# Kernel optimization log

Measured on AMD Instinct MI355X. Metric: run time of the kernel, lower is better.

The kernel has to match this reference:

```python
import jax, jax.numpy as jnp
import numpy as np

N_NODES = 100000
N_EDGES = 1600000


def _sage_conv(x, src, dst, W_l, W_r, b):
    """PyG SAGEConv (mean aggr): lin_l(mean of neighbor feats) + b + lin_r(x)."""
    n = x.shape[0]
    msgs = x[src]                                            # [E, F] gather
    agg = jax.ops.segment_sum(msgs, dst, num_segments=n)     # [N, F]
    cnt = jax.ops.segment_sum(jnp.ones((src.shape[0],), x.dtype), dst,
                              num_segments=n)                # [N]
    mean = agg / jnp.maximum(cnt, 1.0)[:, None]
    return mean @ W_l + b + x @ W_r


def setup_inputs() -> dict:
    key = jax.random.key(0)
    ks = jax.random.split(key, 8)
    x = jax.random.normal(ks[0], (N_NODES, 64), dtype=jnp.float32)
    edge_index = jax.random.randint(ks[1], (2, N_EDGES), 0, N_NODES, dtype=jnp.int64)
    # Glorot-ish small init for weights
    W1_l = jax.random.normal(ks[2], (64, 128), dtype=jnp.float32) * 0.1
    W1_r = jax.random.normal(ks[3], (64, 128), dtype=jnp.float32) * 0.1
    b1 = jax.random.normal(ks[4], (128,), dtype=jnp.float32) * 0.1
    W2_l = jax.random.normal(ks[5], (128, 64), dtype=jnp.float32) * 0.1
    W2_r = jax.random.normal(ks[6], (128, 64), dtype=jnp.float32) * 0.1
    b2 = jax.random.normal(ks[7], (64,), dtype=jnp.float32) * 0.1
    return {"x": x, "edge_index": edge_index, "W1_l": W1_l, "W1_r": W1_r,
            "b1": b1, "W2_l": W2_l, "W2_r": W2_r, "b2": b2}


def reference(x, edge_index, W1_l, W1_r, b1, W2_l, W2_r, b2):
    src, dst = edge_index[0], edge_index[1]
    h = jax.nn.relu(_sage_conv(x, src, dst, W1_l, W1_r, b1))  # [N, 128]
    out = _sage_conv(h, src, dst, W2_l, W2_r, b2)             # [N, 64]
    return out
```

## Files before the change

kernel.cpp:

```cpp
#include <hip/hip_runtime.h>
#include <hip/hip_bf16.h>
#include <stdint.h>


typedef unsigned short u16;
typedef __attribute__((ext_vector_type(8))) short short8;
typedef __attribute__((ext_vector_type(4))) float f32x4;

#define BSHIFT 9
#define BSIZE  512
#define CHUNK  8192
#define NBP    512
#define NCMAX  256

__device__ __forceinline__ float bf2f(u16 v) { return __uint_as_float(((uint32_t)v) << 16); }
__device__ __forceinline__ float bfu_lo(uint32_t u) { return __uint_as_float(u << 16); }
__device__ __forceinline__ float bfu_hi(uint32_t u) { return __uint_as_float(u & 0xffff0000u); }
__device__ __forceinline__ u16 f2bf(float f) {
    uint32_t u = __float_as_uint(f);
    return (u16)((u + 0x7fffu + ((u >> 16) & 1u)) >> 16);
}

__device__ __forceinline__ int wave_scan(int v) {
    int lane = threadIdx.x & 63;
#pragma unroll
    for (int d = 1; d < 64; d <<= 1) {
        int t = __shfl_up(v, d);
        if (lane >= d) v += t;
    }
    return v;
}

__device__ __forceinline__ int block_scan512(int v, int* ws, int* ptot) {
    int tid = threadIdx.x, lane = tid & 63, wid = tid >> 6;
    int s = wave_scan(v);
    if (lane == 63) ws[wid] = s;
    __syncthreads();
    int add = 0, tot = 0;
#pragma unroll
    for (int w = 0; w < 8; w++) { int x = ws[w]; tot += x; if (w < wid) add += x; }
    if (ptot) *ptot = tot;
    __syncthreads();
    return s + add;
}

__global__ __launch_bounds__(512) void setup_k(
    const void* __restrict__ x, const void* __restrict__ ei,
    const void* __restrict__ W1l, const void* __restrict__ W1r,
    const void* __restrict__ b1, const void* __restrict__ W2l,
    const void* __restrict__ W2r, const void* __restrict__ b2,
    u16* __restrict__ wpk, u16* __restrict__ xb,
    int* __restrict__ hist2d, int* __restrict__ flags,
    int nn, int ne, int nb, int nchunk, int ncvt,
    int c0, int c1, int c2, int c3, int c4, int c5, int c6) {
    __shared__ int sh[512];
    __shared__ int sflag;
    int bid = blockIdx.x, tid = threadIdx.x;
    if (bid < nchunk) {
        sh[tid] = 0;
        int samp = 0;
        if (tid < 32) {
            long long n32 = 2LL * ne;
            long long stride = n32 / 32; if (stride < 1) stride = 1;
            long long i = (long long)tid * stride; i |= 1;
            if (i >= n32) i = 1;
            samp = (((const int*)ei)[i] != 0);
        }
        unsigned long long m = __ballot(samp);
        if (tid == 0) sflag = (m == 0ULL) ? 1 : 0;
        __syncthreads();
        int e64 = sflag;
        int base = bid * CHUNK;
#pragma unroll
        for (int j = 0; j < 16; j++) {
            int e = base + j * 512 + tid;
            if (e < ne) {
                int dst = e64 ? (int)((const long long*)ei)[(size_t)ne + e]
                              : ((const int*)ei)[(size_t)ne + e];
                if ((unsigned)dst < (unsigned)nn) atomicAdd(&sh[dst >> BSHIFT], 1);
            }
        }
        __syncthreads();
        if (tid < NBP) hist2d[bid * NBP + tid] = (tid < nb) ? sh[tid] : 0;
    } else if (bid < nchunk + ncvt) {
        int samp = 0;
        if (tid < 32) {
            int C = c0; int stride = C / 32; if (stride < 1) stride = 1;
            long long i = (long long)tid * stride;
            if (i > C - 1) i = C - 1; i &= ~1LL;
            u16 v = ((const u16*)x)[i];
            int e = (v >> 7) & 0xFF;
            samp = ((e >= 0x50 && e <= 0x97) || v == 0) ? 1 : 0;
        }
        unsigned long long m = __ballot(samp);
        if (tid == 0) sflag = (__popcll(m) >= 24) ? 1 : 0;
        __syncthreads();
        if (sflag) return;
        int i = (bid - nchunk) * 512 + tid;
        if (i < nn * 16) {
            float4 f = ((const float4*)x)[i];
            *(ushort4*)&xb[(size_t)i * 4] =
                make_ushort4(f2bf(f.x), f2bf(f.y), f2bf(f.z), f2bf(f.w));
        }
    } else if (bid < nchunk + ncvt + 4) {
        int b = bid - nchunk - ncvt;
        const void* src = (b == 0) ? W1l : (b == 1) ? W1r : (b == 2) ? W2l : W2r;
        int C = (b == 0) ? c1 : (b == 1) ? c2 : (b == 2) ? c4 : c5;
        int samp = 0;
        if (tid < 32) {
            int stride = C / 32; if (stride < 1) stride = 1;
            long long i = (long long)tid * stride;
            if (i > C - 1) i = C - 1; i &= ~1LL;
            u16 v = ((const u16*)src)[i];
            int e = (v >> 7) & 0xFF;
            samp = ((e >= 0x50 && e <= 0x97) || v == 0) ? 1 : 0;
        }
        unsigned long long m = __ballot(samp);
        if (tid == 0) sflag = (__popcll(m) >= 24) ? 1 : 0;
        __syncthreads();
        int isbf = sflag;
        u16* dst = wpk + ((b >= 2) ? (16384 + (b - 2) * 8192) : 0);
        for (int i = tid; i < 2048; i += 512) {
            u16 v0, v1, v2, v3;
            if (isbf) {
                ushort4 u = ((const ushort4*)src)[i];
                v0 = u.x; v1 = u.y; v2 = u.z; v3 = u.w;
            } else {
                float4 u = ((const float4*)src)[i];
                v0 = f2bf(u.x); v1 = f2bf(u.y); v2 = f2bf(u.z); v3 = f2bf(u.w);
            }
            int k, n, k8;
            if (b <= 1) { k = i >> 5; n = (i & 31) * 4; k8 = (b == 1 ? 8 : 0) + (k >> 3); }
            else        { k = i >> 4; n = (i & 15) * 4; k8 = k >> 3; }
            int kc = k8 >> 2, q = k8 & 3, w = k & 7;
            int basei = ((n >> 4) * 4 + kc) * 512 + (q * 16 + (n & 15)) * 8 + w;
            dst[basei] = v0; dst[basei + 8] = v1; dst[basei + 16] = v2; dst[basei + 24] = v3;
        }
    } else {
        int a = tid >> 5, lane = tid & 31;
        if (tid < 8) sh[tid] = 0;
        __syncthreads();
        if (a < 7) {
            const void* ptrs[7] = {x, W1l, W1r, b1, W2l, W2r, b2};
            int cs[7] = {c0, c1, c2, c3, c4, c5, c6};
            int C = cs[a];
            int stride = C / 32; if (stride < 1) stride = 1;
            long long i = (long long)lane * stride;
            if (i > C - 1) i = C - 1;
            i &= ~1LL;
            u16 v = ((const u16*)ptrs[a])[i];
            int e = (v >> 7) & 0xFF;
            int sane = ((e >= 0x50 && e <= 0x97) || v == 0) ? 1 : 0;
            atomicAdd(&sh[a], sane);
        } else if (a == 7) {
            long long n32 = 2LL * ne;
            long long stride = n32 / 32; if (stride < 1) stride = 1;
            long long i = (long long)lane * stride; i |= 1;
            if (i >= n32) i = 1;
            int wv = ((const int*)ei)[i];
            atomicAdd(&sh[7], wv != 0 ? 1 : 0);
        }
        __syncthreads();
        if (tid < 7) flags[tid] = (sh[tid] >= 24) ? 1 : 0;
        if (tid == 7) flags[7] = (sh[7] == 0) ? 1 : 0;
    }
}

__global__ __launch_bounds__(512) void partition_k(
    const void* __restrict__ ei, const int* __restrict__ hist2d,
    unsigned* __restrict__ ep, int nn, int ne, int nb, int nchunk) {
    __shared__ unsigned stage[CHUNK];
    __shared__ u16 ab[CHUNK];
    __shared__ int hist[512], exl[512], gbase[512], lcur[512];
    __shared__ int ws[8];
    __shared__ int e64s;
    int tid = threadIdx.x;
    int base = blockIdx.x * CHUNK;
    hist[tid] = 0;
    int samp = 0;
    if (tid < 32) {
        long long n32 = 2LL * ne;
        long long stride = n32 / 32; if (stride < 1) stride = 1;
        long long i = (long long)tid * stride; i |= 1;
        if (i >= n32) i = 1;
        samp = (((const int*)ei)[i] != 0);
    }
    unsigned long long bm = __ballot(samp);
    if (tid == 0) e64s = (bm == 0ULL) ? 1 : 0;
    __syncthreads();
    int e64 = e64s;
    unsigned pk[16]; int bk[16];
#pragma unroll
    for (int j = 0; j < 16; j++) {
        int e = base + j * 512 + tid;
        bk[j] = -1;
        pk[j] = 0;
        if (e < ne) {
            int src, dst;
            if (e64) {
                src = (int)((const long long*)ei)[e];
                dst = (int)((const long long*)ei)[(size_t)ne + e];
            } else {
                src = ((const int*)ei)[e];
                dst = ((const int*)ei)[(size_t)ne + e];
            }
            if ((unsigned)dst < (unsigned)nn) {
                if ((unsigned)src >= (unsigned)nn) src = 0;
                bk[j] = dst >> BSHIFT;
                pk[j] = (unsigned)src | ((unsigned)(dst & (BSIZE - 1)) << 17);
                atomicAdd(&hist[bk[j]], 1);
            }
        }
    }
    __syncthreads();
    int hv = hist[tid];
    int tot;
    int inc1 = block_scan512(hv, ws, &tot);
    int ex = inc1 - hv;
    exl[tid] = ex;
    lcur[tid] = ex;
    int baseb = 0, tbt = 0;
    int mybid = blockIdx.x;
    if (tid < nb) {
        for (int c = 0; c < nchunk; c++) {
            int h = hist2d[c * NBP + tid];
            tbt += h;
            if (c < mybid) baseb += h;
        }
    }
    int inc2 = block_scan512(tbt, ws, nullptr);
    int bo_t = inc2 - tbt;
    gbase[tid] = (tid < nb) ? (bo_t + baseb) : 0;
    __syncthreads();
#pragma unroll
    for (int j = 0; j < 16; j++) {
        if (bk[j] >= 0) {
            int r = atomicAdd(&lcur[bk[j]], 1);
            stage[r] = pk[j];
            ab[r] = (u16)bk[j];
        }
    }
    __syncthreads();
    for (int j = tid; j < tot; j += 512) {
        int b = ab[j];
        ep[gbase[b] + (j - exl[b])] = stage[j];
    }
}

__global__ __launch_bounds__(512) void csr_fill2(
    const unsigned* __restrict__ ep, const int* __restrict__ hist2d,
    int* __restrict__ off, int* __restrict__ cnt, int* __restrict__ esrc,
    int nn, int nb, int nchunk) {
    __shared__ int hist[BSIZE], lcur[BSIZE];
    __shared__ int ws[8];
    __shared__ int s_end, s_cnt;
    int b = blockIdx.x;
    int tid = threadIdx.x;
    int tbt = 0;
    if (tid < nb) {
        for (int c = 0; c < nchunk; c++) tbt += hist2d[c * NBP + tid];
    }
    int incb = block_scan512(tbt, ws, nullptr);
    if (tid == b) { s_end = incb; s_cnt = tbt; }
    hist[tid] = 0;
    __syncthreads();
    int end = s_end;
    int beg = end - s_cnt;
    for (int j = beg + tid; j < end; j += 512)
        atomicAdd(&hist[(ep[j] >> 17) & (BSIZE - 1)], 1);
    __syncthreads();
    int hv = hist[tid];
    int inc = block_scan512(hv, ws, nullptr);
    int ex = beg + inc - hv;
    lcur[tid] = ex;
    int node = b * BSIZE + tid;
    if (node < nn) { off[node] = ex; cnt[node] = hv; }
    __syncthreads();
    for (int j = beg + tid; j < end; j += 512) {
        unsigned p = ep[j];
        int r = atomicAdd(&lcur[(p >> 17) & (BSIZE - 1)], 1);
        esrc[r] = (int)(p & 0x1FFFFu);
    }
}

__global__ __launch_bounds__(512, 8) void layer1(
    const void* __restrict__ x, const u16* __restrict__ xb,
    const int* __restrict__ esrc,
    const int* __restrict__ off, const int* __restrict__ cnt,
    const u16* __restrict__ w1g, const u16* __restrict__ w2lg,
    const u16* __restrict__ w2rg, const void* __restrict__ b1,
    u16* __restrict__ g, u16* __restrict__ rr,
    const int* __restrict__ flags, int nn) {
    __shared__ __align__(16) u16 wA[8 * 512];
    __shared__ float b_s[128];
    int tid = threadIdx.x;
    int node0 = blockIdx.x * 32;

    if (tid < 128) b_s[tid] = flags[3] ? bf2f(((const u16*)b1)[tid]) : ((const float*)b1)[tid];

    int grp = tid >> 4, gl = tid & 15;
    int n = node0 + grp;
    int mtile = grp >> 4, l15m = grp & 15;
    int idx_mean = (mtile * 4 + (gl >> 3)) * 512 + (((gl >> 1) & 3) * 16 + l15m) * 8 + (gl & 1) * 4;
    int idx_x = (mtile * 4 + 2 + (gl >> 3)) * 512 + (((gl >> 1) & 3) * 16 + l15m) * 8 + (gl & 1) * 4;
    const u16* xs = flags[0] ? (const u16*)x : xb;
    if (n < nn) {
        int beg = off[n], deg = cnt[n];
        float a0 = 0.f, a1 = 0.f, a2 = 0.f, a3 = 0.f;
        int i = 0;
        const u16* xbp = xs + gl * 4;
        for (; i + 16 <= deg; i += 16) {
            ushort4 v[16];
#pragma unroll
            for (int j = 0; j < 16; j++) {
                int s0 = esrc[beg + i + j];
                v[j] = *(const ushort4*)(xbp + (size_t)s0 * 64);
            }
#pragma unroll
            for (int j = 0; j < 16; j++) {
                a0 += bf2f(v[j].x); a1 += bf2f(v[j].y);
                a2 += bf2f(v[j].z); a3 += bf2f(v[j].w);
            }
        }
        for (; i + 8 <= deg; i += 8) {
            ushort4 v[8];
#pragma unroll
            for (int j = 0; j < 8; j++) {
                int s0 = esrc[beg + i + j];
                v[j] = *(const ushort4*)(xbp + (size_t)s0 * 64);
            }
#pragma unroll
            for (int j = 0; j < 8; j++) {
                a0 += bf2f(v[j].x); a1 += bf2f(v[j].y);
                a2 += bf2f(v[j].z); a3 += bf2f(v[j].w);
            }
        }
        for (; i < deg; i++) {
            int s0 = esrc[beg + i];
            ushort4 v = *(const ushort4*)(xbp + (size_t)s0 * 64);
            a0 += bf2f(v.x); a1 += bf2f(v.y); a2 += bf2f(v.z); a3 += bf2f(v.w);
        }
        float inv = 1.0f / (float)(deg > 0 ? deg : 1);
        *(ushort4*)&wA[idx_mean] =
            make_ushort4(f2bf(a0 * inv), f2bf(a1 * inv), f2bf(a2 * inv), f2bf(a3 * inv));
        *(ushort4*)&wA[idx_x] = *(const ushort4*)(xs + (size_t)n * 64 + gl * 4);
    } else {
        *(ushort4*)&wA[idx_mean] = make_ushort4(0, 0, 0, 0);
        *(ushort4*)&wA[idx_x] = make_ushort4(0, 0, 0, 0);
    }
    __syncthreads();

    int wv = tid >> 6, lane = tid & 63;
    int l15 = lane & 15, q = lane >> 4;
    f32x4 acc0 = {0.f, 0.f, 0.f, 0.f};
    f32x4 acc1 = {0.f, 0.f, 0.f, 0.f};
#pragma unroll
    for (int kc = 0; kc < 4; kc++) {
        short8 a0 = *(const short8*)&wA[(kc) * 512 + lane * 8];
        short8 a1 = *(const short8*)&wA[(4 + kc) * 512 + lane * 8];
        short8 b  = *(const short8*)&w1g[(wv * 4 + kc) * 512 + lane * 8];
        acc0 = __builtin_amdgcn_mfma_f32_16x16x32_bf16(a0, b, acc0, 0, 0, 0);
        acc1 = __builtin_amdgcn_mfma_f32_16x16x32_bf16(a1, b, acc1, 0, 0, 0);
    }
    int nc = wv * 16 + l15;
    float bias = b_s[nc];
    u16 hv0[4], hv1[4];
#pragma unroll
    for (int r = 0; r < 4; r++) {
        hv0[r] = f2bf(fmaxf(acc0[r] + bias, 0.0f));
        hv1[r] = f2bf(fmaxf(acc1[r] + bias, 0.0f));
    }
    __syncthreads();
    int kcg = wv >> 1;
    int qg  = ((wv & 1) << 1) | (l15 >> 3);
    int wg  = l15 & 7;
#pragma unroll
    for (int r = 0; r < 4; r++) {
        int m = q * 4 + r;
        wA[kcg * 512 + (qg * 16 + m) * 8 + wg]       = hv0[r];
        wA[(4 + kcg) * 512 + (qg * 16 + m) * 8 + wg] = hv1[r];
    }
    __syncthreads();
    int mt2 = wv >> 2, nt2 = wv & 3;
    f32x4 ag = {0.f, 0.f, 0.f, 0.f};
    f32x4 ar = {0.f, 0.f, 0.f, 0.f};
#pragma unroll
    for (int kc = 0; kc < 4; kc++) {
        short8 a = *(const short8*)&wA[(mt2 * 4 + kc) * 512 + lane * 8];
        short8 bl = *(const short8*)&w2lg[(nt2 * 4 + kc) * 512 + lane * 8];
        short8 br = *(const short8*)&w2rg[(nt2 * 4 + kc) * 512 + lane * 8];
        ag = __builtin_amdgcn_mfma_f32_16x16x32_bf16(a, bl, ag, 0, 0, 0);
        ar = __builtin_amdgcn_mfma_f32_16x16x32_bf16(a, br, ar, 0, 0, 0);
    }
    __syncthreads();
    int nc2 = nt2 * 16 + l15;
#pragma unroll
    for (int r = 0; r < 4; r++) {
        int m = mt2 * 16 + q * 4 + r;
        wA[m * 64 + nc2]        = f2bf(ag[r]);
        wA[2048 + m * 64 + nc2] = f2bf(ar[r]);
    }
    __syncthreads();
    int half = tid >> 8, idx = tid & 255;
    int row = idx >> 3, seg = idx & 7;
    int nd = node0 + row;
    if (nd < nn) {
        uint4 v = *(const uint4*)&wA[half * 2048 + row * 64 + seg * 8];
        u16* dst = (half ? rr : g) + (size_t)nd * 64 + seg * 8;
        *(uint4*)dst = v;
    }
}

__global__ __launch_bounds__(512, 8) void layer2(
    const u16* __restrict__ g, const u16* __restrict__ rr,
    const int* __restrict__ esrc,
    const int* __restrict__ off, const int* __restrict__ cnt,
    const void* __restrict__ b2, void* __restrict__ out,
    const int* __restrict__ flags, int nn) {
    __shared__ float b_s[64];
    int tid = threadIdx.x;
    int node0 = blockIdx.x * 32;
    int obf = flags[0];
    if (tid < 64) b_s[tid] = flags[6] ? bf2f(((const u16*)b2)[tid]) : ((const float*)b2)[tid];
    __syncthreads();

    int grp = tid >> 4, gl = tid & 15;
    int n = node0 + grp;
    if (n >= nn) return;
    int beg = off[n], deg = cnt[n];
    float a0 = 0.f, a1 = 0.f, a2 = 0.f, a3 = 0.f;
    const u16* gb = g + gl * 4;
    int i = 0;
    for (; i + 16 <= deg; i += 16) {
        uint2 v[16];
#pragma unroll
        for (int j = 0; j < 16; j++) {
            int s0 = esrc[beg + i + j];
            v[j] = *(const uint2*)(gb + (size_t)s0 * 64);
        }
#pragma unroll
        for (int j = 0; j < 16; j++) {
            a0 += bfu_lo(v[j].x); a1 += bfu_hi(v[j].x);
            a2 += bfu_lo(v[j].y); a3 += bfu_hi(v[j].y);
        }
    }
    for (; i + 8 <= deg; i += 8) {
        uint2 v[8];
#pragma unroll
        for (int j = 0; j < 8; j++) {
            int s0 = esrc[beg + i + j];
            v[j] = *(const uint2*)(gb + (size_t)s0 * 64);
        }
#pragma unroll
        for (int j = 0; j < 8; j++) {
            a0 += bfu_lo(v[j].x); a1 += bfu_hi(v[j].x);
            a2 += bfu_lo(v[j].y); a3 += bfu_hi(v[j].y);
        }
    }
    for (; i < deg; i++) {
        int s0 = esrc[beg + i];
        uint2 v = *(const uint2*)(gb + (size_t)s0 * 64);
        a0 += bfu_lo(v.x); a1 += bfu_hi(v.x);
        a2 += bfu_lo(v.y); a3 += bfu_hi(v.y);
    }
    float inv = 1.0f / (float)(deg > 0 ? deg : 1);
    uint2 rv = *(const uint2*)(rr + (size_t)n * 64 + gl * 4);
    float o0 = a0 * inv + bfu_lo(rv.x) + b_s[gl * 4 + 0];
    float o1 = a1 * inv + bfu_hi(rv.x) + b_s[gl * 4 + 1];
    float o2 = a2 * inv + bfu_lo(rv.y) + b_s[gl * 4 + 2];
    float o3 = a3 * inv + bfu_hi(rv.y) + b_s[gl * 4 + 3];
    if (obf) {
        u16* op = (u16*)out + (size_t)n * 64 + gl * 4;
        *(ushort4*)op = make_ushort4(f2bf(o0), f2bf(o1), f2bf(o2), f2bf(o3));
    } else {
        float* op = (float*)out + (size_t)n * 64 + gl * 4;
        *(float4*)op = make_float4(o0, o1, o2, o3);
    }
}

__global__ __launch_bounds__(256) void zero_out_k(u16* __restrict__ out, int n) {
    int i = blockIdx.x * 256 + threadIdx.x;
    if (i < n) out[i] = 0;
}

extern "C" void kernel_launch(void* const* d_in, const int* in_sizes, int n_in,
                              void* d_out, int out_size, void* d_ws, size_t ws_size,
                              hipStream_t stream) {
    const void* x   = d_in[0];
    const void* ei  = d_in[1];
    const void* W1l = d_in[2];
    const void* W1r = d_in[3];
    const void* b1  = d_in[4];
    const void* W2l = d_in[5];
    const void* W2r = d_in[6];
    const void* b2  = d_in[7];

    int nn = in_sizes[0] / 64;
    int ne = in_sizes[1] / 2;
    int nb = (nn + BSIZE - 1) / BSIZE;
    int nchunk = (ne + CHUNK - 1) / CHUNK;

    auto al = [](size_t v) { return (v + 255) & ~(size_t)255; };
    size_t o_flags = 0;
    size_t o_wpk   = 256;
    size_t o_cnt   = al(o_wpk + 65536);
    size_t o_off   = al(o_cnt + (size_t)nn * 4);
    size_t o_esrc  = al(o_off + (size_t)nn * 4);
    size_t o_r     = al(o_esrc + (size_t)ne * 4);
    size_t o_xb    = al(o_r + (size_t)nn * 64 * 2);
    size_t o_g     = al(o_xb + (size_t)nn * 64 * 2);
    size_t ws_req  = o_g + (size_t)nn * 64 * 2;

    size_t o_ep   = o_r;
    size_t o_h2d  = al(o_ep + (size_t)ne * 4);
    size_t ov_end = o_h2d + (size_t)NCMAX * NBP * 4;

    bool ok = ws_size >= ws_req && nb >= 1 && nb <= 512 && nn <= 131072 &&
              nchunk <= NCMAX && ov_end <= o_xb;
    if (!ok) {
        zero_out_k<<<(out_size + 255) / 256, 256, 0, stream>>>((u16*)d_out, out_size);
        return;
    }

    char* ws = (char*)d_ws;
    int* flags  = (int*)(ws + o_flags);
    u16* wpk    = (u16*)(ws + o_wpk);
    int* cnt    = (int*)(ws + o_cnt);
    int* off    = (int*)(ws + o_off);
    int* esrc   = (int*)(ws + o_esrc);
    u16* rbuf   = (u16*)(ws + o_r);
    u16* xb     = (u16*)(ws + o_xb);
    u16* gbuf   = (u16*)(ws + o_g);
    unsigned* ep = (unsigned*)(ws + o_ep);
    int* hist2d = (int*)(ws + o_h2d);

    int ncvt = (nn * 16 + 511) / 512;
    setup_k<<<nchunk + ncvt + 5, 512, 0, stream>>>(
        x, ei, W1l, W1r, b1, W2l, W2r, b2, wpk, xb, hist2d, flags,
        nn, ne, nb, nchunk, ncvt,
        in_sizes[0], in_sizes[2], in_sizes[3], in_sizes[4],
        in_sizes[5], in_sizes[6], in_sizes[7]);
    partition_k<<<nchunk, 512, 0, stream>>>(ei, hist2d, ep, nn, ne, nb, nchunk);
    csr_fill2<<<nb, 512, 0, stream>>>(ep, hist2d, off, cnt, esrc, nn, nb, nchunk);
    int lb = (nn + 31) / 32;
    layer1<<<lb, 512, 0, stream>>>(x, xb, esrc, off, cnt,
                                   wpk, wpk + 16384, wpk + 24576, b1,
                                   gbuf, rbuf, flags, nn);
    layer2<<<lb, 512, 0, stream>>>(gbuf, rbuf, esrc, off, cnt, b2, d_out, flags, nn);
}
```

Baseline: 257.4 us.

## Replace two-pass histogram partition with atomic bucket reservation and overflow list

Removes the per-chunk histogram pass over destination indices and its cross-chunk prefix sums. Partition blocks now reserve space in fixed-capacity per-bucket segments through global atomics and write edges straight there, spilling to an overflow list that csr_fill2 re-reads from the edge array. This saves one full read of the edge destinations and the shared-memory staging, in exchange for global atomic contention, scattered writes, and a bucket-count limit lowered to 256. Edge order within a bucket becomes nondeterministic.

```diff
diff --git a/kernel.cpp b/kernel.cpp
--- a/kernel.cpp
+++ b/kernel.cpp
@@ -10,7 +10,6 @@
 #define BSHIFT 9
 #define BSIZE  512
 #define CHUNK  8192
-#define NBP    512
 #define NCMAX  256
 
 __device__ __forceinline__ float bf2f(u16 v) { return __uint_as_float(((uint32_t)v) << 16); }
@@ -50,39 +49,14 @@
     const void* __restrict__ b1, const void* __restrict__ W2l,
     const void* __restrict__ W2r, const void* __restrict__ b2,
     u16* __restrict__ wpk, u16* __restrict__ xb,
-    int* __restrict__ hist2d, int* __restrict__ flags,
-    int nn, int ne, int nb, int nchunk, int ncvt,
+    int* __restrict__ gcur, int* __restrict__ ovfc,
+    int* __restrict__ flags,
+    int nn, int ne, int ncvt,
     int c0, int c1, int c2, int c3, int c4, int c5, int c6) {
-    __shared__ int sh[512];
+    __shared__ int sh[8];
     __shared__ int sflag;
     int bid = blockIdx.x, tid = threadIdx.x;
-    if (bid < nchunk) {
-        sh[tid] = 0;
-        int samp = 0;
-        if (tid < 32) {
-            long long n32 = 2LL * ne;
-            long long stride = n32 / 32; if (stride < 1) stride = 1;
-            long long i = (long long)tid * stride; i |= 1;
-            if (i >= n32) i = 1;
-            samp = (((const int*)ei)[i] != 0);
-        }
-        unsigned long long m = __ballot(samp);
-        if (tid == 0) sflag = (m == 0ULL) ? 1 : 0;
-        __syncthreads();
-        int e64 = sflag;
-        int base = bid * CHUNK;
-#pragma unroll
-        for (int j = 0; j < 16; j++) {
-            int e = base + j * 512 + tid;
-            if (e < ne) {
-                int dst = e64 ? (int)((const long long*)ei)[(size_t)ne + e]
-                              : ((const int*)ei)[(size_t)ne + e];
-                if ((unsigned)dst < (unsigned)nn) atomicAdd(&sh[dst >> BSHIFT], 1);
-            }
-        }
-        __syncthreads();
-        if (tid < NBP) hist2d[bid * NBP + tid] = (tid < nb) ? sh[tid] : 0;
-    } else if (bid < nchunk + ncvt) {
+    if (bid < ncvt) {
         int samp = 0;
         if (tid < 32) {
             int C = c0; int stride = C / 32; if (stride < 1) stride = 1;
@@ -96,14 +70,14 @@
         if (tid == 0) sflag = (__popcll(m) >= 24) ? 1 : 0;
         __syncthreads();
         if (sflag) return;
-        int i = (bid - nchunk) * 512 + tid;
+        int i = bid * 512 + tid;
         if (i < nn * 16) {
             float4 f = ((const float4*)x)[i];
             *(ushort4*)&xb[(size_t)i * 4] =
                 make_ushort4(f2bf(f.x), f2bf(f.y), f2bf(f.z), f2bf(f.w));
         }
-    } else if (bid < nchunk + ncvt + 4) {
-        int b = bid - nchunk - ncvt;
+    } else if (bid < ncvt + 4) {
+        int b = bid - ncvt;
         const void* src = (b == 0) ? W1l : (b == 1) ? W1r : (b == 2) ? W2l : W2r;
         int C = (b == 0) ? c1 : (b == 1) ? c2 : (b == 2) ? c4 : c5;
         int samp = 0;
@@ -137,6 +111,8 @@
             dst[basei] = v0; dst[basei + 8] = v1; dst[basei + 16] = v2; dst[basei + 24] = v3;
         }
     } else {
+        gcur[tid] = 0;
+        if (tid == 0) *ovfc = 0;
         int a = tid >> 5, lane = tid & 31;
         if (tid < 8) sh[tid] = 0;
         __syncthreads();
@@ -167,12 +143,10 @@
 }
 
 __global__ __launch_bounds__(512) void partition_k(
-    const void* __restrict__ ei, const int* __restrict__ hist2d,
-    unsigned* __restrict__ ep, int nn, int ne, int nb, int nchunk) {
-    __shared__ unsigned stage[CHUNK];
-    __shared__ u16 ab[CHUNK];
-    __shared__ int hist[512], exl[512], gbase[512], lcur[512];
-    __shared__ int ws[8];
+    const void* __restrict__ ei, int* __restrict__ gcur,
+    unsigned* __restrict__ ep, unsigned* __restrict__ ovf,
+    int* __restrict__ ovfc, int nn, int ne, int nb, int cap) {
+    __shared__ int hist[512], lcur[512];
     __shared__ int e64s;
     int tid = threadIdx.x;
     int base = blockIdx.x * CHUNK;
@@ -213,61 +187,64 @@
         }
     }
     __syncthreads();
-    int hv = hist[tid];
-    int tot;
-    int inc1 = block_scan512(hv, ws, &tot);
-    int ex = inc1 - hv;
-    exl[tid] = ex;
-    lcur[tid] = ex;
-    int baseb = 0, tbt = 0;
-    int mybid = blockIdx.x;
-    if (tid < nb) {
-        for (int c = 0; c < nchunk; c++) {
-            int h = hist2d[c * NBP + tid];
-            tbt += h;
-            if (c < mybid) baseb += h;
-        }
-    }
-    int inc2 = block_scan512(tbt, ws, nullptr);
-    int bo_t = inc2 - tbt;
-    gbase[tid] = (tid < nb) ? (bo_t + baseb) : 0;
+    lcur[tid] = (tid < nb && hist[tid] > 0) ? atomicAdd(&gcur[tid], hist[tid]) : 0;
     __syncthreads();
 #pragma unroll
     for (int j = 0; j < 16; j++) {
         if (bk[j] >= 0) {
             int r = atomicAdd(&lcur[bk[j]], 1);
-            stage[r] = pk[j];
-            ab[r] = (u16)bk[j];
-        }
-    }
-    __syncthreads();
-    for (int j = tid; j < tot; j += 512) {
-        int b = ab[j];
-        ep[gbase[b] + (j - exl[b])] = stage[j];
+            if (r < cap) {
+                ep[(size_t)bk[j] * cap + r] = pk[j];
+            } else {
+                int oi = atomicAdd(ovfc, 1);
+                ovf[oi] = (unsigned)(base + j * 512 + tid);
+            }
+        }
     }
 }
 
 __global__ __launch_bounds__(512) void csr_fill2(
-    const unsigned* __restrict__ ep, const int* __restrict__ hist2d,
+    const unsigned* __restrict__ ep, const int* __restrict__ gcur,
+    const void* __restrict__ ei, const unsigned* __restrict__ ovf,
+    const int* __restrict__ ovfc,
     int* __restrict__ off, int* __restrict__ cnt, int* __restrict__ esrc,
-    int nn, int nb, int nchunk) {
+    int nn, int ne, int nb, int cap) {
     __shared__ int hist[BSIZE], lcur[BSIZE];
     __shared__ int ws[8];
-    __shared__ int s_end, s_cnt;
+    __shared__ int s_beg;
+    __shared__ int e64s;
     int b = blockIdx.x;
     int tid = threadIdx.x;
-    int tbt = 0;
-    if (tid < nb) {
-        for (int c = 0; c < nchunk; c++) tbt += hist2d[c * NBP + tid];
-    }
-    int incb = block_scan512(tbt, ws, nullptr);
-    if (tid == b) { s_end = incb; s_cnt = tbt; }
+    int samp = 0;
+    if (tid < 32) {
+        long long n32 = 2LL * ne;
+        long long stride = n32 / 32; if (stride < 1) stride = 1;
+        long long i = (long long)tid * stride; i |= 1;
+        if (i >= n32) i = 1;
+        samp = (((const int*)ei)[i] != 0);
+    }
+    unsigned long long bm = __ballot(samp);
+    if (tid == 0) e64s = (bm == 0ULL) ? 1 : 0;
+    int bt = (tid < nb) ? gcur[tid] : 0;
+    int incb = block_scan512(bt, ws, nullptr);
+    if (tid == b) s_beg = incb - bt;
     hist[tid] = 0;
     __syncthreads();
-    int end = s_end;
-    int beg = end - s_cnt;
-    for (int j = beg + tid; j < end; j += 512)
-        atomicAdd(&hist[(ep[j] >> 17) & (BSIZE - 1)], 1);
+    int e64 = e64s;
+    int beg = s_beg;
+    int mytot = gcur[b];
+    int seglen = mytot < cap ? mytot : cap;
+    const unsigned* seg = ep + (size_t)b * cap;
+    for (int j = tid; j < seglen; j += 512)
+        atomicAdd(&hist[(seg[j] >> 17) & (BSIZE - 1)], 1);
+    int no = *ovfc;
+    for (int j = tid; j < no; j += 512) {
+        int e = (int)ovf[j];
+        int dst = e64 ? (int)((const long long*)ei)[(size_t)ne + e]
+                      : ((const int*)ei)[(size_t)ne + e];
+        if ((unsigned)dst < (unsigned)nn && (dst >> BSHIFT) == b)
+            atomicAdd(&hist[dst & (BSIZE - 1)], 1);
+    }
     __syncthreads();
     int hv = hist[tid];
     int inc = block_scan512(hv, ws, nullptr);
@@ -276,10 +253,26 @@
     int node = b * BSIZE + tid;
     if (node < nn) { off[node] = ex; cnt[node] = hv; }
     __syncthreads();
-    for (int j = beg + tid; j < end; j += 512) {
-        unsigned p = ep[j];
+    for (int j = tid; j < seglen; j += 512) {
+        unsigned p = seg[j];
         int r = atomicAdd(&lcur[(p >> 17) & (BSIZE - 1)], 1);
         esrc[r] = (int)(p & 0x1FFFFu);
+    }
+    for (int j = tid; j < no; j += 512) {
+        int e = (int)ovf[j];
+        int src, dst;
+        if (e64) {
+            src = (int)((const long long*)ei)[e];
+            dst = (int)((const long long*)ei)[(size_t)ne + e];
+        } else {
+            src = ((const int*)ei)[e];
+            dst = ((const int*)ei)[(size_t)ne + e];
+        }
+        if ((unsigned)dst < (unsigned)nn && (dst >> BSHIFT) == b) {
+            if ((unsigned)src >= (unsigned)nn) src = 0;
+            int r = atomicAdd(&lcur[dst & (BSIZE - 1)], 1);
+            esrc[r] = src;
+        }
     }
 }
 
@@ -499,10 +492,13 @@
     int ne = in_sizes[1] / 2;
     int nb = (nn + BSIZE - 1) / BSIZE;
     int nchunk = (ne + CHUNK - 1) / CHUNK;
+    int cap = ne / (nb > 0 ? nb : 1) + 4096;
 
     auto al = [](size_t v) { return (v + 255) & ~(size_t)255; };
     size_t o_flags = 0;
-    size_t o_wpk   = 256;
+    size_t o_gcur  = 256;
+    size_t o_ovfc  = o_gcur + 512 * 4;
+    size_t o_wpk   = al(o_ovfc + 4);
     size_t o_cnt   = al(o_wpk + 65536);
     size_t o_off   = al(o_cnt + (size_t)nn * 4);
     size_t o_esrc  = al(o_off + (size_t)nn * 4);
@@ -512,11 +508,12 @@
     size_t ws_req  = o_g + (size_t)nn * 64 * 2;
 
     size_t o_ep   = o_r;
-    size_t o_h2d  = al(o_ep + (size_t)ne * 4);
-    size_t ov_end = o_h2d + (size_t)NCMAX * NBP * 4;
-
-    bool ok = ws_size >= ws_req && nb >= 1 && nb <= 512 && nn <= 131072 &&
-              nchunk <= NCMAX && ov_end <= o_xb;
+    size_t ep_end = o_ep + (size_t)nb * cap * 4;
+    size_t o_ovf  = o_g;
+    size_t ovf_end = o_ovf + (size_t)ne * 4;
+
+    bool ok = ws_size >= ws_req && nb >= 1 && nb <= 256 && nn <= 131072 &&
+              nchunk <= NCMAX && ep_end <= o_xb && ovf_end <= ws_req;
     if (!ok) {
         zero_out_k<<<(out_size + 255) / 256, 256, 0, stream>>>((u16*)d_out, out_size);
         return;
@@ -524,6 +521,8 @@
 
     char* ws = (char*)d_ws;
     int* flags  = (int*)(ws + o_flags);
+    int* gcur   = (int*)(ws + o_gcur);
+    int* ovfc   = (int*)(ws + o_ovfc);
     u16* wpk    = (u16*)(ws + o_wpk);
     int* cnt    = (int*)(ws + o_cnt);
     int* off    = (int*)(ws + o_off);
@@ -531,17 +530,19 @@
     u16* rbuf   = (u16*)(ws + o_r);
     u16* xb     = (u16*)(ws + o_xb);
     u16* gbuf   = (u16*)(ws + o_g);
-    unsigned* ep = (unsigned*)(ws + o_ep);
-    int* hist2d = (int*)(ws + o_h2d);
+    unsigned* ep  = (unsigned*)(ws + o_ep);
+    unsigned* ovf = (unsigned*)(ws + o_ovf);
 
     int ncvt = (nn * 16 + 511) / 512;
-    setup_k<<<nchunk + ncvt + 5, 512, 0, stream>>>(
-        x, ei, W1l, W1r, b1, W2l, W2r, b2, wpk, xb, hist2d, flags,
-        nn, ne, nb, nchunk, ncvt,
+    setup_k<<<ncvt + 5, 512, 0, stream>>>(
+        x, ei, W1l, W1r, b1, W2l, W2r, b2, wpk, xb, gcur, ovfc, flags,
+        nn, ne, ncvt,
         in_sizes[0], in_sizes[2], in_sizes[3], in_sizes[4],
         in_sizes[5], in_sizes[6], in_sizes[7]);
-    partition_k<<<nchunk, 512, 0, stream>>>(ei, hist2d, ep, nn, ne, nb, nchunk);
-    csr_fill2<<<nb, 512, 0, stream>>>(ep, hist2d, off, cnt, esrc, nn, nb, nchunk);
+    partition_k<<<nchunk, 512, 0, stream>>>(ei, gcur, ep, ovf, ovfc,
+                                            nn, ne, nb, cap);
+    csr_fill2<<<nb, 512, 0, stream>>>(ep, gcur, ei, ovf, ovfc,
+                                      off, cnt, esrc, nn, ne, nb, cap);
     int lb = (nn + 31) / 32;
     layer1<<<lb, 512, 0, stream>>>(x, xb, esrc, off, cnt,
                                    wpk, wpk + 16384, wpk + 24576, b1,
```

Result: faster. 225.8 us (-12.3%).
